# Kernel optimization log

Measured on AMD Instinct MI355X. Metric: run time of the kernel, lower is better.

Reference implementation:

```python
import jax, jax.numpy as jnp
import numpy as np

B, N, HS = 2, 2048, 1024
H, D = 16, 64
GRID = 16           # crop_size // patch_size
SEG = 20            # d_dim = h_dim = w_dim = 2*(64//3//2)


def setup_inputs() -> dict:
    key = jax.random.key(0)
    ks = jax.random.split(key, 5)
    s = 0.02
    return {
        "hidden_states": jax.random.normal(ks[0], (B, N, HS), jnp.float32),
        "Wq": jax.random.normal(ks[1], (HS, HS), jnp.float32) * s,
        "bq": jnp.zeros((HS,), jnp.float32),
        "Wk": jax.random.normal(ks[2], (HS, HS), jnp.float32) * s,
        "bk": jnp.zeros((HS,), jnp.float32),
        "Wv": jax.random.normal(ks[3], (HS, HS), jnp.float32) * s,
        "bv": jnp.zeros((HS,), jnp.float32),
        "Wp": jax.random.normal(ks[4], (HS, HS), jnp.float32) * s,
        "bp": jnp.zeros((HS,), jnp.float32),
    }


def _rope(x, pos):
    # x: [B, H, N, d], pos: [N] int. Faithful to rotate_queries_or_keys:
    # sin/cos are TILED (concat of two copies), rotation is pairwise interleaved.
    d = x.shape[-1]
    omega = 1.0 / (10000.0 ** (jnp.arange(d // 2, dtype=x.dtype) / (d / 2.0)))
    freq = pos.astype(x.dtype)[:, None] * omega          # [N, d/2]
    sin = jnp.tile(jnp.sin(freq), (1, 2))                # [N, d]
    cos = jnp.tile(jnp.cos(freq), (1, 2))
    xp = x.reshape(x.shape[:-1] + (d // 2, 2))
    rot = jnp.stack([-xp[..., 1], xp[..., 0]], axis=-1).reshape(x.shape)
    return x * cos + rot * sin


def _apply_rope3d(qk, fpos, hpos, wpos):
    parts, s = [], 0
    for pos in (fpos, hpos, wpos):
        parts.append(_rope(qk[..., s:s + SEG], pos))
        s += SEG
    parts.append(qk[..., s:])  # pass-through remainder (4 dims)
    return jnp.concatenate(parts, axis=-1)


def reference(hidden_states, Wq, bq, Wk, bk, Wv, bv, Wp, bp):
    b, n, _ = hidden_states.shape

    def heads(x):  # [B,N,HS] -> [B,H,N,D]
        return x.reshape(b, n, H, D).transpose(0, 2, 1, 3)

    q = heads(hidden_states @ Wq.T + bq)
    k = heads(hidden_states @ Wk.T + bk)
    v = heads(hidden_states @ Wv.T + bv)

    ids = jnp.arange(n)
    tpf = GRID * GRID
    fpos = ids // tpf
    rem = ids - fpos * tpf
    hpos = rem // GRID
    wpos = rem - hpos * GRID

    q = _apply_rope3d(q, fpos, hpos, wpos)
    k = _apply_rope3d(k, fpos, hpos, wpos)

    scores = jnp.einsum('bhqd,bhkd->bhqk', q, k) * (D ** -0.5)
    probs = jax.nn.softmax(scores.astype(jnp.float32), axis=-1).astype(q.dtype)
    ctx = jnp.einsum('bhqk,bhkd->bqhd', probs, v).reshape(b, n, HS)
    return ctx @ Wp.T + bp
```

## Files before the change

### kernel.cpp

```cpp
#include <hip/hip_runtime.h>
#include <hip/hip_bf16.h>
#include <math.h>

#define BB    2
#define NN    2048
#define HSZ   1024
#define NH    16
#define HD    64
#define SEGW  20

#define LOG2E  1.4426950408889634f
#define QSCALE (0.125f * LOG2E)
#define DTHR   8.0f

typedef unsigned short u16;
typedef unsigned int   u32;
using bf16x8 = __attribute__((ext_vector_type(8))) short;
using f32x4  = __attribute__((ext_vector_type(4))) float;

__device__ __forceinline__ u16 f2b(float f) {
    union { float f; u32 u; } x; x.f = f;
    u32 r = x.u + 0x7FFF + ((x.u >> 16) & 1);
    return (u16)(r >> 16);
}
__device__ __forceinline__ u16 f2bc(float f) {
    __hip_bfloat16 h = __float2bfloat16(f);
    return *reinterpret_cast<u16*>(&h);
}

__device__ __forceinline__ void gload16(void* lds, const void* g) {
    __builtin_amdgcn_global_load_lds(
        (const __attribute__((address_space(1))) void*)g,
        (__attribute__((address_space(3))) void*)lds, 16, 0, 0);
}

__global__ __launch_bounds__(256)
void cast_k(const float* __restrict__ hs, const float* __restrict__ Wq,
            const float* __restrict__ Wk, const float* __restrict__ Wv,
            const float* __restrict__ Wp, u16* __restrict__ hsb,
            u16* __restrict__ wqb, u16* __restrict__ wkb,
            u16* __restrict__ wvb, u16* __restrict__ wpb) {
    size_t idx = ((size_t)blockIdx.x * 256 + threadIdx.x) * 4;
    const float* s; u16* d; size_t o;
    const size_t HSN = 4194304, WN = 1048576;
    if      (idx < HSN)          { s = hs; d = hsb; o = idx; }
    else if (idx < HSN + WN)     { s = Wq; d = wqb; o = idx - HSN; }
    else if (idx < HSN + 2*WN)   { s = Wk; d = wkb; o = idx - HSN - WN; }
    else if (idx < HSN + 3*WN)   { s = Wv; d = wvb; o = idx - HSN - 2*WN; }
    else                         { s = Wp; d = wpb; o = idx - HSN - 3*WN; }
    float4 v = *(const float4*)(s + o);
    u32 lo = f2b(v.x) | ((u32)f2b(v.y) << 16);
    u32 hi = f2b(v.z) | ((u32)f2b(v.w) << 16);
    *(uint2*)(d + o) = uint2{lo, hi};
}

__global__ void rope_table_k(float* __restrict__ tab) {
    int n = blockIdx.x, d = threadIdx.x;
    float c = 1.f, s = 0.f;
    if (d < 3 * SEGW) {
        int seg = d / SEGW;
        int jj  = (d % SEGW) % (SEGW / 2);
        int rem = n & 255;
        int pos = (seg == 0) ? (n >> 8) : ((seg == 1) ? (rem >> 4) : (rem & 15));
        float omega = powf(10000.f, -(float)jj / 10.f);
        float fr = (float)pos * omega;
        s = sinf(fr); c = cosf(fr);
    }
    tab[(n * 64 + d) * 2 + 0] = c;
    tab[(n * 64 + d) * 2 + 1] = s;
}

__device__ __forceinline__
void gemm_body(const u16* __restrict__ X, const u16* __restrict__ Wb,
               const float* __restrict__ bias, void* __restrict__ out,
               const float* __restrict__ tab, int mode) {
    __shared__ u16 As[2][128 * 32];
    __shared__ u16 Bs[2][64 * 32];

    const int t  = threadIdx.x;
    const int w  = t >> 6;
    const int l  = t & 63;
    const int o0 = blockIdx.x * 64;
    const int m0 = blockIdx.y * 128;
    const int wr = (w >> 1) * 64;
    const int wc = (w & 1) * 32;

    const int chA0 = (w << 6) + l;
    const int rA0 = chA0 >> 2,         cA0 = (chA0 & 3) * 8;
    const int rA1 = (chA0 + 256) >> 2, cA1 = (chA0 & 3) * 8;
    const int rB  = chA0 >> 2,         cB  = (chA0 & 3) * 8;

    f32x4 acc[4][2] = {};

    gload16(As[0] + ((w << 6)) * 8,       X  + (size_t)(m0 + rA0) * HSZ + cA0);
    gload16(As[0] + (256 + (w << 6)) * 8, X  + (size_t)(m0 + rA1) * HSZ + cA1);
    gload16(Bs[0] + ((w << 6)) * 8,       Wb + (size_t)(o0 + rB) * HSZ + cB);
    __syncthreads();

    int cur = 0;
    for (int k0 = 0; k0 < HSZ; k0 += 32, cur ^= 1) {
        if (k0 + 32 < HSZ) {
            int kn = k0 + 32;
            gload16(As[cur ^ 1] + ((w << 6)) * 8,       X  + (size_t)(m0 + rA0) * HSZ + kn + cA0);
            gload16(As[cur ^ 1] + (256 + (w << 6)) * 8, X  + (size_t)(m0 + rA1) * HSZ + kn + cA1);
            gload16(Bs[cur ^ 1] + ((w << 6)) * 8,       Wb + (size_t)(o0 + rB) * HSZ + kn + cB);
        }
        bf16x8 af[4], bfr[2];
#pragma unroll
        for (int i = 0; i < 4; ++i)
            af[i] = *(const bf16x8*)(As[cur] + (wr + i * 16 + (l & 15)) * 32 + (l >> 4) * 8);
#pragma unroll
        for (int j = 0; j < 2; ++j)
            bfr[j] = *(const bf16x8*)(Bs[cur] + (wc + j * 16 + (l & 15)) * 32 + (l >> 4) * 8);
#pragma unroll
        for (int i = 0; i < 4; ++i)
#pragma unroll
            for (int j = 0; j < 2; ++j)
                acc[i][j] = __builtin_amdgcn_mfma_f32_16x16x32_bf16(af[i], bfr[j], acc[i][j], 0, 0, 0);
        __syncthreads();
    }

    const int h = o0 >> 6;
#pragma unroll
    for (int ct = 0; ct < 2; ++ct) {
        int oc = o0 + wc + ct * 16 + (l & 15);
        int d  = oc & 63;
        float bv = bias[oc];
        if (mode == 2) {
#pragma unroll
            for (int rt = 0; rt < 4; ++rt) {
                int base = m0 + wr + rt * 16 + (l >> 4) * 4;
                int b_ = base >> 11, n0 = base & (NN - 1);
                u16 e[4];
#pragma unroll
                for (int r = 0; r < 4; ++r) e[r] = f2b(acc[rt][ct][r] + bv);
                u32 lo = e[0] | ((u32)e[1] << 16);
                u32 hi = e[2] | ((u32)e[3] << 16);
                u16* vp = (u16*)out + (((size_t)b_ * NH + h) * HD + d) * NN + n0;
                *(uint2*)vp = uint2{lo, hi};
            }
        } else if (mode == 3) {
#pragma unroll
            for (int rt = 0; rt < 4; ++rt)
#pragma unroll
                for (int r = 0; r < 4; ++r) {
                    int m = m0 + wr + rt * 16 + (l >> 4) * 4 + r;
                    ((float*)out)[(size_t)m * HSZ + oc] = acc[rt][ct][r] + bv;
                }
        } else {
            float scl = (mode == 0) ? QSCALE : 1.f;
#pragma unroll
            for (int rt = 0; rt < 4; ++rt)
#pragma unroll
                for (int r = 0; r < 4; ++r) {
                    int m = m0 + wr + rt * 16 + (l >> 4) * 4 + r;
                    int n = m & (NN - 1), b_ = m >> 11;
                    float v = acc[rt][ct][r] + bv;
                    float2 cs = ((const float2*)tab)[n * 64 + d];
                    float part = __shfl_xor(v, 1);
                    float vr = (l & 1) ? fmaf(part, cs.y, v * cs.x)
                                       : fmaf(-part, cs.y, v * cs.x);
                    u16* qp = (u16*)out + (((size_t)b_ * NH + h) * NN + n) * HD + d;
                    *qp = f2b(vr * scl);
                }
        }
    }
}

__global__ __launch_bounds__(256)
void qkv_k(const u16* __restrict__ X,
           const u16* __restrict__ Wq, const u16* __restrict__ Wk, const u16* __restrict__ Wv,
           const float* __restrict__ bq, const float* __restrict__ bk, const float* __restrict__ bv,
           u16* __restrict__ qo, u16* __restrict__ ko, u16* __restrict__ vo,
           const float* __restrict__ tab) {
    int z = blockIdx.z;
    const u16* W   = (z == 0) ? Wq : (z == 1) ? Wk : Wv;
    const float* b = (z == 0) ? bq : (z == 1) ? bk : bv;
    u16* o         = (z == 0) ? qo : (z == 1) ? ko : vo;
    gemm_body(X, W, b, o, tab, z);
}

__global__ __launch_bounds__(256)
void projo_k(const u16* __restrict__ X, const u16* __restrict__ W,
             const float* __restrict__ b, float* __restrict__ out) {
    gemm_body(X, W, b, out, nullptr, 3);
}

__global__ __launch_bounds__(256)
void attn_mfma_k(const u16* __restrict__ Qb, const u16* __restrict__ Kb,
                 const u16* __restrict__ Vtb, u16* __restrict__ ctxb) {
    __shared__ u16 QPs[64 * 64];
    __shared__ u16 Ks[2][64 * 64];
    __shared__ u16 Vs[2][64 * 64];

    const int t = threadIdx.x, w = t >> 6, l = t & 63;
    int f   = blockIdx.y * 32 + blockIdx.x;
    int bh  = (f & 7) * 4 + ((f >> 3) & 3);
    int qt  = f >> 5;
    const int b_ = bh >> 4, h = bh & 15;

    const u16* Qg  = Qb + ((size_t)bh * NN + qt * 64) * HD;
    const u16* Kg0 = Kb + (size_t)bh * NN * HD;
    const u16* Vg0 = Vtb + (size_t)bh * HD * NN;

    const int ch0 = (w << 6) + l;
    const int r0 = ch0 >> 3,         s0 = (ch0 & 7) ^ (r0 & 7);
    const int r1 = (ch0 + 256) >> 3, s1 = (ch0 & 7) ^ (r1 & 7);

    gload16(QPs + ((w << 6)) * 8,       Qg + r0 * HD + s0 * 8);
    gload16(QPs + (256 + (w << 6)) * 8, Qg + r1 * HD + s1 * 8);
    gload16(Ks[0] + ((w << 6)) * 8,       Kg0 + (size_t)r0 * HD + s0 * 8);
    gload16(Ks[0] + (256 + (w << 6)) * 8, Kg0 + (size_t)r1 * HD + s1 * 8);
    gload16(Vs[0] + ((w << 6)) * 8,       Vg0 + (size_t)r0 * NN + s0 * 8);
    gload16(Vs[0] + (256 + (w << 6)) * 8, Vg0 + (size_t)r1 * NN + s1 * 8);
    __syncthreads();

    bf16x8 qf[2];
#pragma unroll
    for (int kk = 0; kk < 2; ++kk) {
        int row = w * 16 + (l & 15);
        int cb = (kk * 64 + (l >> 4) * 16) ^ ((row & 7) << 4);
        qf[kk] = *(const bf16x8*)((const char*)QPs + row * 128 + cb);
    }
    __syncthreads();

    bf16x8 ones;
#pragma unroll
    for (int i = 0; i < 8; ++i) ones[i] = (short)0x3F80;

    float m_i[4] = {-INFINITY, -INFINITY, -INFINITY, -INFINITY};
    float l_i[4] = {};
    f32x4 o_acc[4] = {};

    int cur = 0;
    for (int kt = 0; kt < NN / 64; ++kt, cur ^= 1) {
        if (kt + 1 < NN / 64) {
            const u16* Kg = Kg0 + (size_t)((kt + 1) * 64) * HD;
            const u16* Vg = Vg0 + (kt + 1) * 64;
            gload16(Ks[cur ^ 1] + ((w << 6)) * 8,       Kg + (size_t)r0 * HD + s0 * 8);
            gload16(Ks[cur ^ 1] + (256 + (w << 6)) * 8, Kg + (size_t)r1 * HD + s1 * 8);
            gload16(Vs[cur ^ 1] + ((w << 6)) * 8,       Vg + (size_t)r0 * NN + s0 * 8);
            gload16(Vs[cur ^ 1] + (256 + (w << 6)) * 8, Vg + (size_t)r1 * NN + s1 * 8);
        }

        f32x4 sacc[4] = {};
        __builtin_amdgcn_s_setprio(1);
#pragma unroll
        for (int ct = 0; ct < 4; ++ct)
#pragma unroll
            for (int kk = 0; kk < 2; ++kk) {
                int row = ct * 16 + (l & 15);
                int cb = (kk * 64 + (l >> 4) * 16) ^ ((row & 7) << 4);
                bf16x8 kf = *(const bf16x8*)((const char*)Ks[cur] + row * 128 + cb);
                sacc[ct] = __builtin_amdgcn_mfma_f32_16x16x32_bf16(qf[kk], kf, sacc[ct], 0, 0, 0);
            }
        __builtin_amdgcn_s_setprio(0);

        float pm[4];
#pragma unroll
        for (int r = 0; r < 4; ++r)
            pm[r] = fmaxf(fmaxf(sacc[0][r], sacc[1][r]), fmaxf(sacc[2][r], sacc[3][r]));
        bool grow = (pm[0] > m_i[0] + DTHR) | (pm[1] > m_i[1] + DTHR) |
                    (pm[2] > m_i[2] + DTHR) | (pm[3] > m_i[3] + DTHR);
        if (__any(grow)) {
#pragma unroll
            for (int r = 0; r < 4; ++r) {
                float mx = pm[r];
                mx = fmaxf(mx, __shfl_xor(mx, 1));
                mx = fmaxf(mx, __shfl_xor(mx, 2));
                mx = fmaxf(mx, __shfl_xor(mx, 4));
                mx = fmaxf(mx, __shfl_xor(mx, 8));
                float mn = fmaxf(m_i[r], mx);
                float alpha = __builtin_amdgcn_exp2f(m_i[r] - mn);
                m_i[r] = mn;
                l_i[r] *= alpha;
#pragma unroll
                for (int dt = 0; dt < 4; ++dt) o_acc[dt][r] *= alpha;
            }
        }

#pragma unroll
        for (int ct = 0; ct < 4; ++ct)
#pragma unroll
            for (int r = 0; r < 4; ++r) {
                float p = __builtin_amdgcn_exp2f(sacc[ct][r] - m_i[r]);
                int row = w * 16 + (l >> 4) * 4 + r;
                int cb = ((ct * 16 + (l & 15)) * 2) ^ ((row & 7) << 4);
                *(u16*)((char*)QPs + row * 128 + cb) = f2bc(p);
            }

        f32x4 lacc = {};
        __builtin_amdgcn_s_setprio(1);
#pragma unroll
        for (int kk = 0; kk < 2; ++kk) {
            int prow = w * 16 + (l & 15);
            int pcb = (kk * 64 + (l >> 4) * 16) ^ ((prow & 7) << 4);
            bf16x8 pf = *(const bf16x8*)((const char*)QPs + prow * 128 + pcb);
            lacc = __builtin_amdgcn_mfma_f32_16x16x32_bf16(pf, ones, lacc, 0, 0, 0);
#pragma unroll
            for (int dt = 0; dt < 4; ++dt) {
                int vrow = dt * 16 + (l & 15);
                int vcb = (kk * 64 + (l >> 4) * 16) ^ ((vrow & 7) << 4);
                bf16x8 vf = *(const bf16x8*)((const char*)Vs[cur] + vrow * 128 + vcb);
                o_acc[dt] = __builtin_amdgcn_mfma_f32_16x16x32_bf16(pf, vf, o_acc[dt], 0, 0, 0);
            }
        }
        __builtin_amdgcn_s_setprio(0);
#pragma unroll
        for (int r = 0; r < 4; ++r) l_i[r] += lacc[r];

        __syncthreads();
    }

#pragma unroll
    for (int r = 0; r < 4; ++r) {
        float inv = 1.f / l_i[r];
        int n = qt * 64 + w * 16 + (l >> 4) * 4 + r;
#pragma unroll
        for (int dt = 0; dt < 4; ++dt) {
            int d = dt * 16 + (l & 15);
            ctxb[((size_t)b_ * NN + n) * HSZ + h * HD + d] = f2bc(o_acc[dt][r] * inv);
        }
    }
}

extern "C" void kernel_launch(void* const* d_in, const int* in_sizes, int n_in,
                              void* d_out, int out_size, void* d_ws, size_t ws_size,
                              hipStream_t stream) {
    (void)in_sizes; (void)n_in; (void)out_size; (void)ws_size;
    const float* hs = (const float*)d_in[0];
    const float* Wq = (const float*)d_in[1];
    const float* bq = (const float*)d_in[2];
    const float* Wk = (const float*)d_in[3];
    const float* bk = (const float*)d_in[4];
    const float* Wv = (const float*)d_in[5];
    const float* bv = (const float*)d_in[6];
    const float* Wp = (const float*)d_in[7];
    const float* bp = (const float*)d_in[8];

    char* ws = (char*)d_ws;
    u16*   hsb  = (u16*)(ws);
    u16*   Wqb  = (u16*)(ws + 8388608);
    u16*   Wkb  = (u16*)(ws + 10485760);
    u16*   Wvb  = (u16*)(ws + 12582912);
    u16*   Wpb  = (u16*)(ws + 14680064);
    u16*   qb   = (u16*)(ws + 16777216);
    u16*   kb   = (u16*)(ws + 25165824);
    u16*   vtb  = (u16*)(ws + 33554432);
    u16*   ctxb = (u16*)(ws + 41943040);
    float* tab  = (float*)(ws + 50331648);

    cast_k<<<8192, 256, 0, stream>>>(hs, Wq, Wk, Wv, Wp, hsb, Wqb, Wkb, Wvb, Wpb);
    rope_table_k<<<NN, 64, 0, stream>>>(tab);

    qkv_k<<<dim3(HSZ / 64, (BB * NN) / 128, 3), 256, 0, stream>>>(
        hsb, Wqb, Wkb, Wvb, bq, bk, bv, qb, kb, vtb, tab);

    attn_mfma_k<<<dim3(NN / 64, BB * NH), 256, 0, stream>>>(qb, kb, vtb, ctxb);

    projo_k<<<dim3(HSZ / 64, (BB * NN) / 128), 256, 0, stream>>>(ctxb, Wpb, bp, (float*)d_out);
}
```

Baseline: 159.7 us.

## Enlarge GEMM and attention tiles to 128x128 and 128 queries, swizzle GEMM LDS

The GEMM tile grows from 128x64 to 128x128, so each wave computes 4x4 MFMA tiles, and the LDS layout gets an XOR swizzle to avoid bank conflicts. The attention kernel now handles 128 query rows per block, two 16-row slices per wave, so each K/V tile loaded into LDS is reused across twice as many queries. Both changes raise arithmetic intensity and cut global and LDS traffic per flop. In exchange they use more registers and LDS and launch half as many blocks, which may lower occupancy and leave fewer waves per CU on a 256-CU part.

```diff
diff --git a/kernel.cpp b/kernel.cpp
--- a/kernel.cpp
+++ b/kernel.cpp
@@ -75,26 +75,27 @@
                const float* __restrict__ bias, void* __restrict__ out,
                const float* __restrict__ tab, int mode) {
     __shared__ u16 As[2][128 * 32];
-    __shared__ u16 Bs[2][64 * 32];
+    __shared__ u16 Bs[2][128 * 32];
 
     const int t  = threadIdx.x;
     const int w  = t >> 6;
     const int l  = t & 63;
-    const int o0 = blockIdx.x * 64;
+    const int o0 = blockIdx.x * 128;
     const int m0 = blockIdx.y * 128;
     const int wr = (w >> 1) * 64;
-    const int wc = (w & 1) * 32;
-
-    const int chA0 = (w << 6) + l;
-    const int rA0 = chA0 >> 2,         cA0 = (chA0 & 3) * 8;
-    const int rA1 = (chA0 + 256) >> 2, cA1 = (chA0 & 3) * 8;
-    const int rB  = chA0 >> 2,         cB  = (chA0 & 3) * 8;
-
-    f32x4 acc[4][2] = {};
+    const int wc = (w & 1) * 64;
+
+    const int ch  = (w << 6) + l;
+    const int rA0 = ch >> 2,         cA0 = (((ch & 3) ^ (rA0 & 3))) * 8;
+    const int rA1 = (ch + 256) >> 2, cA1 = (((ch & 3) ^ (rA1 & 3))) * 8;
+    const int kbyte = (((l >> 4) ^ (l & 3)) << 4);
+
+    f32x4 acc[4][4] = {};
 
     gload16(As[0] + ((w << 6)) * 8,       X  + (size_t)(m0 + rA0) * HSZ + cA0);
     gload16(As[0] + (256 + (w << 6)) * 8, X  + (size_t)(m0 + rA1) * HSZ + cA1);
-    gload16(Bs[0] + ((w << 6)) * 8,       Wb + (size_t)(o0 + rB) * HSZ + cB);
+    gload16(Bs[0] + ((w << 6)) * 8,       Wb + (size_t)(o0 + rA0) * HSZ + cA0);
+    gload16(Bs[0] + (256 + (w << 6)) * 8, Wb + (size_t)(o0 + rA1) * HSZ + cA1);
     __syncthreads();
 
     int cur = 0;
@@ -103,27 +104,34 @@
             int kn = k0 + 32;
             gload16(As[cur ^ 1] + ((w << 6)) * 8,       X  + (size_t)(m0 + rA0) * HSZ + kn + cA0);
             gload16(As[cur ^ 1] + (256 + (w << 6)) * 8, X  + (size_t)(m0 + rA1) * HSZ + kn + cA1);
-            gload16(Bs[cur ^ 1] + ((w << 6)) * 8,       Wb + (size_t)(o0 + rB) * HSZ + kn + cB);
-        }
-        bf16x8 af[4], bfr[2];
+            gload16(Bs[cur ^ 1] + ((w << 6)) * 8,       Wb + (size_t)(o0 + rA0) * HSZ + kn + cA0);
+            gload16(Bs[cur ^ 1] + (256 + (w << 6)) * 8, Wb + (size_t)(o0 + rA1) * HSZ + kn + cA1);
+        }
+        bf16x8 af[4], bfr[4];
+#pragma unroll
+        for (int i = 0; i < 4; ++i) {
+            int row = wr + i * 16 + (l & 15);
+            af[i] = *(const bf16x8*)((const char*)As[cur] + row * 64 + kbyte);
+        }
+#pragma unroll
+        for (int j = 0; j < 4; ++j) {
+            int row = wc + j * 16 + (l & 15);
+            bfr[j] = *(const bf16x8*)((const char*)Bs[cur] + row * 64 + kbyte);
+        }
+        __builtin_amdgcn_s_setprio(1);
 #pragma unroll
         for (int i = 0; i < 4; ++i)
-            af[i] = *(const bf16x8*)(As[cur] + (wr + i * 16 + (l & 15)) * 32 + (l >> 4) * 8);
-#pragma unroll
-        for (int j = 0; j < 2; ++j)
-            bfr[j] = *(const bf16x8*)(Bs[cur] + (wc + j * 16 + (l & 15)) * 32 + (l >> 4) * 8);
-#pragma unroll
-        for (int i = 0; i < 4; ++i)
-#pragma unroll
-            for (int j = 0; j < 2; ++j)
+#pragma unroll
+            for (int j = 0; j < 4; ++j)
                 acc[i][j] = __builtin_amdgcn_mfma_f32_16x16x32_bf16(af[i], bfr[j], acc[i][j], 0, 0, 0);
+        __builtin_amdgcn_s_setprio(0);
         __syncthreads();
     }
 
-    const int h = o0 >> 6;
-#pragma unroll
-    for (int ct = 0; ct < 2; ++ct) {
-        int oc = o0 + wc + ct * 16 + (l & 15);
+#pragma unroll
+    for (int j = 0; j < 4; ++j) {
+        int oc = o0 + wc + j * 16 + (l & 15);
+        int h  = oc >> 6;
         int d  = oc & 63;
         float bv = bias[oc];
         if (mode == 2) {
@@ -133,7 +141,7 @@
                 int b_ = base >> 11, n0 = base & (NN - 1);
                 u16 e[4];
 #pragma unroll
-                for (int r = 0; r < 4; ++r) e[r] = f2b(acc[rt][ct][r] + bv);
+                for (int r = 0; r < 4; ++r) e[r] = f2b(acc[rt][j][r] + bv);
                 u32 lo = e[0] | ((u32)e[1] << 16);
                 u32 hi = e[2] | ((u32)e[3] << 16);
                 u16* vp = (u16*)out + (((size_t)b_ * NH + h) * HD + d) * NN + n0;
@@ -145,7 +153,7 @@
 #pragma unroll
                 for (int r = 0; r < 4; ++r) {
                     int m = m0 + wr + rt * 16 + (l >> 4) * 4 + r;
-                    ((float*)out)[(size_t)m * HSZ + oc] = acc[rt][ct][r] + bv;
+                    ((float*)out)[(size_t)m * HSZ + oc] = acc[rt][j][r] + bv;
                 }
         } else {
             float scl = (mode == 0) ? QSCALE : 1.f;
@@ -155,7 +163,7 @@
                 for (int r = 0; r < 4; ++r) {
                     int m = m0 + wr + rt * 16 + (l >> 4) * 4 + r;
                     int n = m & (NN - 1), b_ = m >> 11;
-                    float v = acc[rt][ct][r] + bv;
+                    float v = acc[rt][j][r] + bv;
                     float2 cs = ((const float2*)tab)[n * 64 + d];
                     float part = __shfl_xor(v, 1);
                     float vr = (l & 1) ? fmaf(part, cs.y, v * cs.x)
@@ -189,17 +197,17 @@
 __global__ __launch_bounds__(256)
 void attn_mfma_k(const u16* __restrict__ Qb, const u16* __restrict__ Kb,
                  const u16* __restrict__ Vtb, u16* __restrict__ ctxb) {
-    __shared__ u16 QPs[64 * 64];
+    __shared__ u16 QPs[128 * 64];
     __shared__ u16 Ks[2][64 * 64];
     __shared__ u16 Vs[2][64 * 64];
 
     const int t = threadIdx.x, w = t >> 6, l = t & 63;
-    int f   = blockIdx.y * 32 + blockIdx.x;
-    int bh  = (f & 7) * 4 + ((f >> 3) & 3);
-    int qt  = f >> 5;
+    int f  = blockIdx.y * 16 + blockIdx.x;
+    int bh = (f & 7) * 4 + ((f >> 3) & 3);
+    int qt = f >> 5;
     const int b_ = bh >> 4, h = bh & 15;
 
-    const u16* Qg  = Qb + ((size_t)bh * NN + qt * 64) * HD;
+    const u16* Qg  = Qb + ((size_t)bh * NN + qt * 128) * HD;
     const u16* Kg0 = Kb + (size_t)bh * NN * HD;
     const u16* Vg0 = Vtb + (size_t)bh * HD * NN;
 
@@ -207,30 +215,39 @@
     const int r0 = ch0 >> 3,         s0 = (ch0 & 7) ^ (r0 & 7);
     const int r1 = (ch0 + 256) >> 3, s1 = (ch0 & 7) ^ (r1 & 7);
 
-    gload16(QPs + ((w << 6)) * 8,       Qg + r0 * HD + s0 * 8);
-    gload16(QPs + (256 + (w << 6)) * 8, Qg + r1 * HD + s1 * 8);
+#pragma unroll
+    for (int s = 0; s < 4; ++s) {
+        int c = s * 256 + ch0;
+        int row = c >> 3, sc = (c & 7) ^ (row & 7);
+        gload16(QPs + (s * 256 + (w << 6)) * 8, Qg + row * HD + sc * 8);
+    }
     gload16(Ks[0] + ((w << 6)) * 8,       Kg0 + (size_t)r0 * HD + s0 * 8);
     gload16(Ks[0] + (256 + (w << 6)) * 8, Kg0 + (size_t)r1 * HD + s1 * 8);
     gload16(Vs[0] + ((w << 6)) * 8,       Vg0 + (size_t)r0 * NN + s0 * 8);
     gload16(Vs[0] + (256 + (w << 6)) * 8, Vg0 + (size_t)r1 * NN + s1 * 8);
     __syncthreads();
 
-    bf16x8 qf[2];
-#pragma unroll
-    for (int kk = 0; kk < 2; ++kk) {
-        int row = w * 16 + (l & 15);
-        int cb = (kk * 64 + (l >> 4) * 16) ^ ((row & 7) << 4);
-        qf[kk] = *(const bf16x8*)((const char*)QPs + row * 128 + cb);
-    }
+    bf16x8 qf[2][2];
+#pragma unroll
+    for (int qs = 0; qs < 2; ++qs)
+#pragma unroll
+        for (int kk = 0; kk < 2; ++kk) {
+            int row = w * 32 + qs * 16 + (l & 15);
+            int cb = (kk * 64 + (l >> 4) * 16) ^ ((row & 7) << 4);
+            qf[qs][kk] = *(const bf16x8*)((const char*)QPs + row * 128 + cb);
+        }
     __syncthreads();
 
     bf16x8 ones;
 #pragma unroll
     for (int i = 0; i < 8; ++i) ones[i] = (short)0x3F80;
 
-    float m_i[4] = {-INFINITY, -INFINITY, -INFINITY, -INFINITY};
-    float l_i[4] = {};
-    f32x4 o_acc[4] = {};
+    float m_i[2][4], l_i[2][4] = {};
+#pragma unroll
+    for (int qs = 0; qs < 2; ++qs)
+#pragma unroll
+        for (int r = 0; r < 4; ++r) m_i[qs][r] = -INFINITY;
+    f32x4 o_acc[2][4] = {};
 
     int cur = 0;
     for (int kt = 0; kt < NN / 64; ++kt, cur ^= 1) {
@@ -243,85 +260,105 @@
             gload16(Vs[cur ^ 1] + (256 + (w << 6)) * 8, Vg + (size_t)r1 * NN + s1 * 8);
         }
 
-        f32x4 sacc[4] = {};
+        f32x4 sacc[2][4] = {};
         __builtin_amdgcn_s_setprio(1);
 #pragma unroll
-        for (int ct = 0; ct < 4; ++ct)
+        for (int ct = 0; ct < 4; ++ct) {
+            int row = ct * 16 + (l & 15);
 #pragma unroll
             for (int kk = 0; kk < 2; ++kk) {
-                int row = ct * 16 + (l & 15);
                 int cb = (kk * 64 + (l >> 4) * 16) ^ ((row & 7) << 4);
                 bf16x8 kf = *(const bf16x8*)((const char*)Ks[cur] + row * 128 + cb);
-                sacc[ct] = __builtin_amdgcn_mfma_f32_16x16x32_bf16(qf[kk], kf, sacc[ct], 0, 0, 0);
-            }
+                sacc[0][ct] = __builtin_amdgcn_mfma_f32_16x16x32_bf16(qf[0][kk], kf, sacc[0][ct], 0, 0, 0);
+                sacc[1][ct] = __builtin_amdgcn_mfma_f32_16x16x32_bf16(qf[1][kk], kf, sacc[1][ct], 0, 0, 0);
+            }
+        }
         __builtin_amdgcn_s_setprio(0);
 
-        float pm[4];
-#pragma unroll
-        for (int r = 0; r < 4; ++r)
-            pm[r] = fmaxf(fmaxf(sacc[0][r], sacc[1][r]), fmaxf(sacc[2][r], sacc[3][r]));
-        bool grow = (pm[0] > m_i[0] + DTHR) | (pm[1] > m_i[1] + DTHR) |
-                    (pm[2] > m_i[2] + DTHR) | (pm[3] > m_i[3] + DTHR);
+        float pm[2][4];
+        bool grow = false;
+#pragma unroll
+        for (int qs = 0; qs < 2; ++qs)
+#pragma unroll
+            for (int r = 0; r < 4; ++r) {
+                pm[qs][r] = fmaxf(fmaxf(sacc[qs][0][r], sacc[qs][1][r]),
+                                  fmaxf(sacc[qs][2][r], sacc[qs][3][r]));
+                grow = grow | (pm[qs][r] > m_i[qs][r] + DTHR);
+            }
         if (__any(grow)) {
 #pragma unroll
-            for (int r = 0; r < 4; ++r) {
-                float mx = pm[r];
-                mx = fmaxf(mx, __shfl_xor(mx, 1));
-                mx = fmaxf(mx, __shfl_xor(mx, 2));
-                mx = fmaxf(mx, __shfl_xor(mx, 4));
-                mx = fmaxf(mx, __shfl_xor(mx, 8));
-                float mn = fmaxf(m_i[r], mx);
-                float alpha = __builtin_amdgcn_exp2f(m_i[r] - mn);
-                m_i[r] = mn;
-                l_i[r] *= alpha;
-#pragma unroll
-                for (int dt = 0; dt < 4; ++dt) o_acc[dt][r] *= alpha;
-            }
-        }
-
-#pragma unroll
-        for (int ct = 0; ct < 4; ++ct)
-#pragma unroll
-            for (int r = 0; r < 4; ++r) {
-                float p = __builtin_amdgcn_exp2f(sacc[ct][r] - m_i[r]);
-                int row = w * 16 + (l >> 4) * 4 + r;
-                int cb = ((ct * 16 + (l & 15)) * 2) ^ ((row & 7) << 4);
-                *(u16*)((char*)QPs + row * 128 + cb) = f2bc(p);
-            }
-
-        f32x4 lacc = {};
+            for (int qs = 0; qs < 2; ++qs)
+#pragma unroll
+                for (int r = 0; r < 4; ++r) {
+                    float mx = pm[qs][r];
+                    mx = fmaxf(mx, __shfl_xor(mx, 1));
+                    mx = fmaxf(mx, __shfl_xor(mx, 2));
+                    mx = fmaxf(mx, __shfl_xor(mx, 4));
+                    mx = fmaxf(mx, __shfl_xor(mx, 8));
+                    float mn = fmaxf(m_i[qs][r], mx);
+                    float alpha = __builtin_amdgcn_exp2f(m_i[qs][r] - mn);
+                    m_i[qs][r] = mn;
+                    l_i[qs][r] *= alpha;
+#pragma unroll
+                    for (int dt = 0; dt < 4; ++dt) o_acc[qs][dt][r] *= alpha;
+                }
+        }
+
+#pragma unroll
+        for (int qs = 0; qs < 2; ++qs)
+#pragma unroll
+            for (int ct = 0; ct < 4; ++ct)
+#pragma unroll
+                for (int r = 0; r < 4; ++r) {
+                    float p = __builtin_amdgcn_exp2f(sacc[qs][ct][r] - m_i[qs][r]);
+                    int row = w * 32 + qs * 16 + (l >> 4) * 4 + r;
+                    int cb = ((ct * 16 + (l & 15)) * 2) ^ ((row & 7) << 4);
+                    *(u16*)((char*)QPs + row * 128 + cb) = f2bc(p);
+                }
+
+        f32x4 lacc[2] = {};
         __builtin_amdgcn_s_setprio(1);
 #pragma unroll
         for (int kk = 0; kk < 2; ++kk) {
-            int prow = w * 16 + (l & 15);
-            int pcb = (kk * 64 + (l >> 4) * 16) ^ ((prow & 7) << 4);
-            bf16x8 pf = *(const bf16x8*)((const char*)QPs + prow * 128 + pcb);
-            lacc = __builtin_amdgcn_mfma_f32_16x16x32_bf16(pf, ones, lacc, 0, 0, 0);
+            bf16x8 pf[2];
+#pragma unroll
+            for (int qs = 0; qs < 2; ++qs) {
+                int prow = w * 32 + qs * 16 + (l & 15);
+                int pcb = (kk * 64 + (l >> 4) * 16) ^ ((prow & 7) << 4);
+                pf[qs] = *(const bf16x8*)((const char*)QPs + prow * 128 + pcb);
+            }
+            lacc[0] = __builtin_amdgcn_mfma_f32_16x16x32_bf16(pf[0], ones, lacc[0], 0, 0, 0);
+            lacc[1] = __builtin_amdgcn_mfma_f32_16x16x32_bf16(pf[1], ones, lacc[1], 0, 0, 0);
 #pragma unroll
             for (int dt = 0; dt < 4; ++dt) {
                 int vrow = dt * 16 + (l & 15);
                 int vcb = (kk * 64 + (l >> 4) * 16) ^ ((vrow & 7) << 4);
                 bf16x8 vf = *(const bf16x8*)((const char*)Vs[cur] + vrow * 128 + vcb);
-                o_acc[dt] = __builtin_amdgcn_mfma_f32_16x16x32_bf16(pf, vf, o_acc[dt], 0, 0, 0);
+                o_acc[0][dt] = __builtin_amdgcn_mfma_f32_16x16x32_bf16(pf[0], vf, o_acc[0][dt], 0, 0, 0);
+                o_acc[1][dt] = __builtin_amdgcn_mfma_f32_16x16x32_bf16(pf[1], vf, o_acc[1][dt], 0, 0, 0);
             }
         }
         __builtin_amdgcn_s_setprio(0);
 #pragma unroll
-        for (int r = 0; r < 4; ++r) l_i[r] += lacc[r];
+        for (int qs = 0; qs < 2; ++qs)
+#pragma unroll
+            for (int r = 0; r < 4; ++r) l_i[qs][r] += lacc[qs][r];
 
         __syncthreads();
     }
 
 #pragma unroll
-    for (int r = 0; r < 4; ++r) {
-        float inv = 1.f / l_i[r];
-        int n = qt * 64 + w * 16 + (l >> 4) * 4 + r;
-#pragma unroll
-        for (int dt = 0; dt < 4; ++dt) {
-            int d = dt * 16 + (l & 15);
-            ctxb[((size_t)b_ * NN + n) * HSZ + h * HD + d] = f2bc(o_acc[dt][r] * inv);
-        }
-    }
+    for (int qs = 0; qs < 2; ++qs)
+#pragma unroll
+        for (int r = 0; r < 4; ++r) {
+            float inv = 1.f / l_i[qs][r];
+            int n = qt * 128 + w * 32 + qs * 16 + (l >> 4) * 4 + r;
+#pragma unroll
+            for (int dt = 0; dt < 4; ++dt) {
+                int d = dt * 16 + (l & 15);
+                ctxb[((size_t)b_ * NN + n) * HSZ + h * HD + d] = f2bc(o_acc[qs][dt][r] * inv);
+            }
+        }
 }
 
 extern "C" void kernel_launch(void* const* d_in, const int* in_sizes, int n_in,
@@ -353,10 +390,10 @@
     cast_k<<<8192, 256, 0, stream>>>(hs, Wq, Wk, Wv, Wp, hsb, Wqb, Wkb, Wvb, Wpb);
     rope_table_k<<<NN, 64, 0, stream>>>(tab);
 
-    qkv_k<<<dim3(HSZ / 64, (BB * NN) / 128, 3), 256, 0, stream>>>(
+    qkv_k<<<dim3(HSZ / 128, (BB * NN) / 128, 3), 256, 0, stream>>>(
         hsb, Wqb, Wkb, Wvb, bq, bk, bv, qb, kb, vtb, tab);
 
-    attn_mfma_k<<<dim3(NN / 64, BB * NH), 256, 0, stream>>>(qb, kb, vtb, ctxb);
-
-    projo_k<<<dim3(HSZ / 64, (BB * NN) / 128), 256, 0, stream>>>(ctxb, Wpb, bp, (float*)d_out);
-}
+    attn_mfma_k<<<dim3(NN / 128, BB * NH), 256, 0, stream>>>(qb, kb, vtb, ctxb);
+
+    projo_k<<<dim3(HSZ / 128, (BB * NN) / 128), 256, 0, stream>>>(ctxb, Wpb, bp, (float*)d_out);
+}
```

New measurement: 150.9 us. 1.06x faster.
